# Optimization experiments

Measured on AMD Instinct MI355X. Metric: run time of the kernel, lower is better.

The kernel has to match this reference:

```python
import jax, jax.numpy as jnp
import numpy as np

N_NODES = 100_000
N_EDGES = 1_600_000
N_TOKENS = 16
VOCAB = 32_000
TOK_DIM = 64
NODE_DIM = 64
HID = 128
FC = 128
NUM_GRAPHS = 1024


def setup_inputs() -> dict:
    key = jax.random.key(0)
    ks = jax.random.split(key, 14)
    emb = jax.random.normal(ks[0], (VOCAB, TOK_DIM), jnp.float32) * 0.02
    emb = emb.at[0].set(0.0)  # padding_idx=0 row is zero
    return {
        "x_token_idxs": jax.random.randint(ks[1], (N_NODES, N_TOKENS), 0, VOCAB),
        "edge_index": jax.random.randint(ks[2], (2, N_EDGES), 0, N_NODES),
        "batch": jnp.sort(jax.random.randint(ks[3], (N_NODES,), 0, NUM_GRAPHS)),
        "emb": emb,
        "Wp": jax.random.normal(ks[4], (TOK_DIM, NODE_DIM), jnp.float32) * (1.0 / np.sqrt(TOK_DIM)),
        "bp": jnp.zeros((NODE_DIM,), jnp.float32),
        "W1": jax.random.normal(ks[5], (NODE_DIM, HID), jnp.float32) * (1.0 / np.sqrt(NODE_DIM)),
        "b1": jnp.zeros((HID,), jnp.float32),
        "W2": jax.random.normal(ks[6], (HID, HID), jnp.float32) * (1.0 / np.sqrt(HID)),
        "b2": jnp.zeros((HID,), jnp.float32),
        "Wfc": jax.random.normal(ks[7], (HID, FC), jnp.float32) * (1.0 / np.sqrt(HID)),
        "bfc": jnp.zeros((FC,), jnp.float32),
        "Wout": jax.random.normal(ks[8], (FC, 1), jnp.float32) * (1.0 / np.sqrt(FC)),
        "bout": jnp.zeros((1,), jnp.float32),
    }


def reference(x_token_idxs, edge_index, batch, emb, Wp, bp, W1, b1, W2, b2, Wfc, bfc, Wout, bout):
    N = x_token_idxs.shape[0]
    # token embed -> mean pool over tokens -> node projection
    node = emb[x_token_idxs].mean(axis=1) @ Wp + bp  # [N, NODE_DIM]

    # GCN normalization with self-loops (PyG gcn_norm, symmetric)
    loops = jnp.arange(N)
    src = jnp.concatenate([edge_index[0], loops])
    dst = jnp.concatenate([edge_index[1], loops])
    deg = jax.ops.segment_sum(jnp.ones_like(dst, jnp.float32), dst, num_segments=N)
    dis = jnp.where(deg > 0, jax.lax.rsqrt(deg), 0.0)
    norm = (dis[src] * dis[dst])[:, None]  # [E+N, 1]

    def gcn(x, W, b):
        h = x @ W                                      # linear transform first (in->out)
        msg = h[src] * norm                            # gather + scale
        return jax.ops.segment_sum(msg, dst, num_segments=N) + b  # scatter-add + bias

    x = jax.nn.relu(gcn(node, W1, b1))
    x = jax.nn.relu(gcn(x, W2, b2))

    # global mean pool by graph id
    cnt = jax.ops.segment_sum(jnp.ones((N,), jnp.float32), batch, num_segments=NUM_GRAPHS)
    g = jax.ops.segment_sum(x, batch, num_segments=NUM_GRAPHS) / jnp.maximum(cnt, 1.0)[:, None]

    g = jax.nn.relu(g @ Wfc + bfc)
    logits = (g @ Wout + bout).squeeze(-1)  # [NUM_GRAPHS]
    return jax.nn.sigmoid(logits), logits
```

## Files before the change

### kernel.cpp

```cpp
#include <hip/hip_runtime.h>
#include <hip/hip_bf16.h>
#include <hip/hip_fp16.h>
#include <math.h>

#define N_TOKENS 16
#define TOK_DIM 64
#define NODE_DIM 64
#define HID 128
#define FC 128
#define NUM_GRAPHS 1024
#define NBUCK_MAX 512
#define CHUNK 8192

typedef _Float16 f16x8 __attribute__((ext_vector_type(8)));
typedef float f32x4 __attribute__((ext_vector_type(4)));

__device__ __forceinline__ __half2 shfl_xor_h2(__half2 v, int mask) {
    int i = *(int*)&v;
    i = __shfl_xor(i, mask);
    return *(__half2*)&i;
}

__global__ void prep_weights_kernel(const float* __restrict__ Wp, const float* __restrict__ W1,
                                    const float* __restrict__ W2, const float* __restrict__ bp,
                                    _Float16* __restrict__ Wf16t, _Float16* __restrict__ W2t,
                                    float* __restrict__ bf) {
    int n = blockIdx.x;
    int t = threadIdx.x;
    if (t < 64) {
        float acc = 0.f;
#pragma unroll
        for (int d = 0; d < 64; d++) acc += Wp[t * 64 + d] * W1[d * 128 + n];
        Wf16t[(size_t)n * 64 + t] = (_Float16)acc;
    } else {
        int d = t - 64;
        float v = bp[d] * W1[d * 128 + n];
#pragma unroll
        for (int off = 32; off > 0; off >>= 1) v += __shfl_down(v, off);
        if (d == 0) bf[n] = v;
    }
    W2t[(size_t)n * 128 + t] = (_Float16)W2[(size_t)t * 128 + n];
}

__global__ void convert_emb_kernel(const float* __restrict__ emb, __half* __restrict__ emb16,
                                   int n4) {
    int i = blockIdx.x * 256 + threadIdx.x;
    if (i < n4) {
        float4 v = ((const float4*)emb)[i];
        __half2 h0 = __floats2half2_rn(v.x, v.y);
        __half2 h1 = __floats2half2_rn(v.z, v.w);
        float2 p;
        ((__half2*)&p)[0] = h0;
        ((__half2*)&p)[1] = h1;
        ((float2*)emb16)[i] = p;
    }
}

__global__ void embed_mean_kernel(const int* __restrict__ tok,
                                  const __half* __restrict__ emb16,
                                  __half* __restrict__ mean16, int N) {
    int t = threadIdx.x;
    int w = t >> 6, j = t & 63;
    int q = j >> 3, l = j & 7;
    int i = blockIdx.x * 4 + w;
    if (i >= N) return;
    const float4* e4 = (const float4*)emb16;
    int t0 = tok[i * 16 + q];
    int t1 = tok[i * 16 + q + 8];
    float4 v0 = e4[(size_t)t0 * 8 + l];
    float4 v1 = e4[(size_t)t1 * 8 + l];
    const __half2* p0 = (const __half2*)&v0;
    const __half2* p1 = (const __half2*)&v1;
    __half2 a0 = __hadd2(p0[0], p1[0]);
    __half2 a1 = __hadd2(p0[1], p1[1]);
    __half2 a2 = __hadd2(p0[2], p1[2]);
    __half2 a3 = __hadd2(p0[3], p1[3]);
#pragma unroll
    for (int mask = 8; mask <= 32; mask <<= 1) {
        a0 = __hadd2(a0, shfl_xor_h2(a0, mask));
        a1 = __hadd2(a1, shfl_xor_h2(a1, mask));
        a2 = __hadd2(a2, shfl_xor_h2(a2, mask));
        a3 = __hadd2(a3, shfl_xor_h2(a3, mask));
    }
    if (q == 0) {
        __half2 inv = __floats2half2_rn(1.0f / 16.0f, 1.0f / 16.0f);
        float4 packed;
        __half2* pp = (__half2*)&packed;
        pp[0] = __hmul2(a0, inv);
        pp[1] = __hmul2(a1, inv);
        pp[2] = __hmul2(a2, inv);
        pp[3] = __hmul2(a3, inv);
        ((float4*)mean16)[(size_t)i * 8 + l] = packed;
    }
}

__global__ void bucket_hist_kernel(const int* __restrict__ dst, int* __restrict__ bucket_cnt,
                                   int E, int nbuck) {
    __shared__ int h[NBUCK_MAX];
    int t = threadIdx.x;
    for (int i = t; i < nbuck; i += 512) h[i] = 0;
    __syncthreads();
    int base = blockIdx.x * CHUNK;
    for (int i = t; i < CHUNK; i += 512) {
        int e = base + i;
        if (e < E) atomicAdd(&h[dst[e] >> 8], 1);
    }
    __syncthreads();
    for (int i = t; i < nbuck; i += 512)
        if (h[i]) atomicAdd(&bucket_cnt[i], h[i]);
}

__global__ void bucket_scan_kernel(const int* __restrict__ bucket_cnt,
                                   int* __restrict__ bucket_base,
                                   int* __restrict__ bucket_cursor, int nbuck) {
    __shared__ int s[512];
    int tid = threadIdx.x;
    int v = (tid < nbuck) ? bucket_cnt[tid] : 0;
    s[tid] = v;
    __syncthreads();
    for (int off = 1; off < 512; off <<= 1) {
        int add = (tid >= off) ? s[tid - off] : 0;
        __syncthreads();
        s[tid] += add;
        __syncthreads();
    }
    if (tid < nbuck) { bucket_base[tid] = s[tid] - v; bucket_cursor[tid] = 0; }
    if (tid == 511) bucket_base[nbuck] = s[511];
}

__global__ void binscatter_kernel(const int* __restrict__ src, const int* __restrict__ dst,
                                  const int* __restrict__ bucket_base,
                                  int* __restrict__ bucket_cursor,
                                  int* __restrict__ staged, int E, int nbuck) {
    __shared__ int h[NBUCK_MAX];
    __shared__ int gw[NBUCK_MAX];
    int t = threadIdx.x;
    for (int i = t; i < nbuck; i += 512) h[i] = 0;
    __syncthreads();
    int base = blockIdx.x * CHUNK;
    for (int i = t; i < CHUNK; i += 512) {
        int e = base + i;
        if (e < E) atomicAdd(&h[dst[e] >> 8], 1);
    }
    __syncthreads();
    for (int i = t; i < nbuck; i += 512) {
        int c = h[i];
        gw[i] = (c > 0) ? bucket_base[i] + atomicAdd(&bucket_cursor[i], c) : 0;
        h[i] = 0;
    }
    __syncthreads();
    for (int i = t; i < CHUNK; i += 512) {
        int e = base + i;
        if (e < E) {
            int d = dst[e], s = src[e];
            int b = d >> 8;
            int r = atomicAdd(&h[b], 1);
            staged[gw[b] + r] = s | ((d & 255) << 17);
        }
    }
}

__global__ void bucket_count_kernel(const int* __restrict__ staged,
                                    const int* __restrict__ bucket_base,
                                    int* __restrict__ row_start, float* __restrict__ dis,
                                    int N, int E) {
    __shared__ int cnt[256];
    __shared__ int sc[256];
    int b = blockIdx.x;
    int t = threadIdx.x;
    cnt[t] = 0;
    __syncthreads();
    int rb0 = bucket_base[b], rb1 = bucket_base[b + 1];
    for (int i = rb0 + t; i < rb1; i += 256) atomicAdd(&cnt[staged[i] >> 17], 1);
    __syncthreads();
    int v = cnt[t];
    sc[t] = v;
    __syncthreads();
    for (int off = 1; off < 256; off <<= 1) {
        int add = (t >= off) ? sc[t - off] : 0;
        __syncthreads();
        sc[t] += add;
        __syncthreads();
    }
    int node = b * 256 + t;
    if (node < N) {
        row_start[node] = rb0 + sc[t] - v;
        dis[node] = rsqrtf(1.0f + (float)v);
    }
    if (b == 0 && t == 0) row_start[N] = E;
}

__global__ void csr_write_kernel(const int* __restrict__ staged,
                                 const int* __restrict__ bucket_base,
                                 const int* __restrict__ row_start,
                                 const float* __restrict__ dis,
                                 int2* __restrict__ csr, float* __restrict__ rowsum, int N) {
    __shared__ int cur[256];
    __shared__ float dl[256];
    __shared__ float wsum[256];
    int b = blockIdx.x;
    int t = threadIdx.x;
    int node = b * 256 + t;
    cur[t] = (node < N) ? row_start[node] : 0;
    dl[t] = (node < N) ? dis[node] : 0.f;
    wsum[t] = 0.f;
    __syncthreads();
    int rb0 = bucket_base[b], rb1 = bucket_base[b + 1];
    for (int i = rb0 + t; i < rb1; i += 256) {
        int v = staged[i];
        int s = v & 131071;
        int dloc = v >> 17;
        float w = dis[s] * dl[dloc];
        int pos = atomicAdd(&cur[dloc], 1);
        __half2 wh = __floats2half2_rn(w, w);
        csr[pos] = make_int2(s, *(int*)&wh);
        atomicAdd(&wsum[dloc], w);
    }
    __syncthreads();
    if (node < N) rowsum[node] = wsum[t] + dl[t] * dl[t];
}

__global__ __launch_bounds__(256, 8)
void agg64_kernel(const __half* __restrict__ mean16,
                  const int* __restrict__ row_start,
                  const int2* __restrict__ csr,
                  const float* __restrict__ dis,
                  __half* __restrict__ agg16, int N) {
    int t = threadIdx.x;
    int w = t >> 6, j = t & 63;
    int q = j >> 3, l = j & 7;
    int node = blockIdx.x * 4 + w;
    if (node >= N) return;
    int beg = row_start[node];
    int end = row_start[node + 1];
    float d = dis[node];
    const float4* m4 = (const float4*)mean16;
    __half2 a0, a1, a2, a3;
    {
        float4 raw = m4[(size_t)node * 8 + l];
        const __half2* hp = (const __half2*)&raw;
        float d2f = d * d * ((q == 0) ? 1.f : 0.f);
        __half2 d2h = __floats2half2_rn(d2f, d2f);
        a0 = __hmul2(hp[0], d2h); a1 = __hmul2(hp[1], d2h);
        a2 = __hmul2(hp[2], d2h); a3 = __hmul2(hp[3], d2h);
    }
    int k = beg;
    int kfull = beg + ((end - beg) & ~31);
    for (; k < kfull; k += 32) {
        int2 e[4];
        float4 v[4];
#pragma unroll
        for (int m = 0; m < 4; m++) e[m] = csr[k + 8 * m + q];
#pragma unroll
        for (int m = 0; m < 4; m++) v[m] = m4[(size_t)e[m].x * 8 + l];
#pragma unroll
        for (int m = 0; m < 4; m++) {
            __half2 wh = *(__half2*)&e[m].y;
            const __half2* hp = (const __half2*)&v[m];
            a0 = __hfma2(hp[0], wh, a0);
            a1 = __hfma2(hp[1], wh, a1);
            a2 = __hfma2(hp[2], wh, a2);
            a3 = __hfma2(hp[3], wh, a3);
        }
    }
    if (k < end) {
        int2 e[4];
        float4 v[4];
#pragma unroll
        for (int m = 0; m < 4; m++) {
            int kk = k + 8 * m + q;
            e[m] = (kk < end) ? csr[kk] : make_int2(0, 0);
        }
#pragma unroll
        for (int m = 0; m < 4; m++) v[m] = m4[(size_t)e[m].x * 8 + l];
#pragma unroll
        for (int m = 0; m < 4; m++) {
            __half2 wh = *(__half2*)&e[m].y;
            const __half2* hp = (const __half2*)&v[m];
            a0 = __hfma2(hp[0], wh, a0);
            a1 = __hfma2(hp[1], wh, a1);
            a2 = __hfma2(hp[2], wh, a2);
            a3 = __hfma2(hp[3], wh, a3);
        }
    }
#pragma unroll
    for (int mask = 8; mask <= 32; mask <<= 1) {
        a0 = __hadd2(a0, shfl_xor_h2(a0, mask));
        a1 = __hadd2(a1, shfl_xor_h2(a1, mask));
        a2 = __hadd2(a2, shfl_xor_h2(a2, mask));
        a3 = __hadd2(a3, shfl_xor_h2(a3, mask));
    }
    if (q == 0) {
        float4 packed;
        __half2* pp = (__half2*)&packed;
        pp[0] = a0; pp[1] = a1; pp[2] = a2; pp[3] = a3;
        ((float4*)agg16)[(size_t)node * 8 + l] = packed;
    }
}

#define NB 32
__global__ void dense_chain_mfma_kernel(const __half* __restrict__ agg16,
                                        const float* __restrict__ rowsum,
                                        const _Float16* __restrict__ Wf16t,
                                        const float* __restrict__ bf,
                                        const float* __restrict__ b1,
                                        const _Float16* __restrict__ W2t,
                                        __half* __restrict__ h2, int N) {
    __shared__ _Float16 sx1[32][136];
    __shared__ float srs[32];
    int t = threadIdx.x;
    int wv = t >> 6, lane = t & 63;
    int nb0 = blockIdx.x * NB;
    int rh = wv & 1;
    int ncb = (wv >> 1) * 64;
    int m16 = lane & 15;
    int q = lane >> 4;

    if (t < 32) srs[t] = (nb0 + t < N) ? rowsum[nb0 + t] : 0.f;

    f32x4 c0 = {}, c1 = {}, c2 = {}, c3 = {};
    int arow = nb0 + rh * 16 + m16;
    bool rowok = (arow < N);
    const _Float16* ag = (const _Float16*)agg16;
#pragma unroll
    for (int ks = 0; ks < 2; ks++) {
        int k0 = ks * 32 + q * 8;
        f16x8 afrag = {};
        if (rowok) afrag = *(const f16x8*)(ag + (size_t)arow * 64 + k0);
        f16x8 b0 = *(const f16x8*)(Wf16t + (size_t)(ncb + 0 * 16 + m16) * 64 + k0);
        f16x8 b1f = *(const f16x8*)(Wf16t + (size_t)(ncb + 1 * 16 + m16) * 64 + k0);
        f16x8 b2f = *(const f16x8*)(Wf16t + (size_t)(ncb + 2 * 16 + m16) * 64 + k0);
        f16x8 b3f = *(const f16x8*)(Wf16t + (size_t)(ncb + 3 * 16 + m16) * 64 + k0);
        c0 = __builtin_amdgcn_mfma_f32_16x16x32_f16(afrag, b0, c0, 0, 0, 0);
        c1 = __builtin_amdgcn_mfma_f32_16x16x32_f16(afrag, b1f, c1, 0, 0, 0);
        c2 = __builtin_amdgcn_mfma_f32_16x16x32_f16(afrag, b2f, c2, 0, 0, 0);
        c3 = __builtin_amdgcn_mfma_f32_16x16x32_f16(afrag, b3f, c3, 0, 0, 0);
    }
    __syncthreads();
    {
        f32x4 cc[4] = {c0, c1, c2, c3};
#pragma unroll
        for (int nt = 0; nt < 4; nt++) {
            int ncol = ncb + nt * 16 + m16;
            float bfj = bf[ncol], b1j = b1[ncol];
#pragma unroll
            for (int r = 0; r < 4; r++) {
                int mrow = q * 4 + r;
                float z = cc[nt][r] + srs[rh * 16 + mrow] * bfj + b1j;
                sx1[rh * 16 + mrow][ncol] = (_Float16)fmaxf(z, 0.f);
            }
        }
    }
    __syncthreads();

    f32x4 d0 = {}, d1 = {}, d2 = {}, d3 = {};
#pragma unroll
    for (int ks = 0; ks < 4; ks++) {
        int k0 = ks * 32 + q * 8;
        f16x8 afrag = *(const f16x8*)(&sx1[rh * 16 + m16][k0]);
        f16x8 b0 = *(const f16x8*)(W2t + (size_t)(ncb + 0 * 16 + m16) * 128 + k0);
        f16x8 b1f = *(const f16x8*)(W2t + (size_t)(ncb + 1 * 16 + m16) * 128 + k0);
        f16x8 b2f = *(const f16x8*)(W2t + (size_t)(ncb + 2 * 16 + m16) * 128 + k0);
        f16x8 b3f = *(const f16x8*)(W2t + (size_t)(ncb + 3 * 16 + m16) * 128 + k0);
        d0 = __builtin_amdgcn_mfma_f32_16x16x32_f16(afrag, b0, d0, 0, 0, 0);
        d1 = __builtin_amdgcn_mfma_f32_16x16x32_f16(afrag, b1f, d1, 0, 0, 0);
        d2 = __builtin_amdgcn_mfma_f32_16x16x32_f16(afrag, b2f, d2, 0, 0, 0);
        d3 = __builtin_amdgcn_mfma_f32_16x16x32_f16(afrag, b3f, d3, 0, 0, 0);
    }
    {
        f32x4 dd[4] = {d0, d1, d2, d3};
#pragma unroll
        for (int nt = 0; nt < 4; nt++) {
            int ncol = ncb + nt * 16 + m16;
#pragma unroll
            for (int r = 0; r < 4; r++) {
                int node = nb0 + rh * 16 + q * 4 + r;
                if (node < N) h2[(size_t)node * 128 + ncol] = __float2half(dd[nt][r]);
            }
        }
    }
}

__global__ __launch_bounds__(256, 8)
void gcn_agg128_kernel(const __half* __restrict__ hsrc,
                       const int* __restrict__ row_start,
                       const int2* __restrict__ csr,
                       const float* __restrict__ dis,
                       const float* __restrict__ b2,
                       __half* __restrict__ outx, int N) {
    int t = threadIdx.x;
    int w = t >> 6, j = t & 63;
    int q = j >> 4, l = j & 15;
    int node = blockIdx.x * 4 + w;
    if (node >= N) return;
    const float4* h4 = (const float4*)hsrc;
    int beg = row_start[node];
    int end = row_start[node + 1];
    float d = dis[node];
    __half2 a0, a1, a2, a3;
    {
        float4 raw = h4[(size_t)node * 16 + l];
        const __half2* hp = (const __half2*)&raw;
        float d2f = d * d * ((q == 0) ? 1.f : 0.f);
        __half2 d2h = __floats2half2_rn(d2f, d2f);
        a0 = __hmul2(hp[0], d2h); a1 = __hmul2(hp[1], d2h);
        a2 = __hmul2(hp[2], d2h); a3 = __hmul2(hp[3], d2h);
    }
    int k = beg;
    int kfull = beg + ((end - beg) & ~31);
    for (; k < kfull; k += 32) {
        int2 e[8];
        float4 v[8];
#pragma unroll
        for (int m = 0; m < 8; m++) e[m] = csr[k + 4 * m + q];
#pragma unroll
        for (int m = 0; m < 8; m++) v[m] = h4[(size_t)e[m].x * 16 + l];
#pragma unroll
        for (int m = 0; m < 8; m++) {
            __half2 wh = *(__half2*)&e[m].y;
            const __half2* hp = (const __half2*)&v[m];
            a0 = __hfma2(hp[0], wh, a0);
            a1 = __hfma2(hp[1], wh, a1);
            a2 = __hfma2(hp[2], wh, a2);
            a3 = __hfma2(hp[3], wh, a3);
        }
    }
    if (k < end) {
        int2 e[8];
        float4 v[8];
#pragma unroll
        for (int m = 0; m < 8; m++) {
            int kk = k + 4 * m + q;
            e[m] = (kk < end) ? csr[kk] : make_int2(0, 0);
        }
#pragma unroll
        for (int m = 0; m < 8; m++) v[m] = h4[(size_t)e[m].x * 16 + l];
#pragma unroll
        for (int m = 0; m < 8; m++) {
            __half2 wh = *(__half2*)&e[m].y;
            const __half2* hp = (const __half2*)&v[m];
            a0 = __hfma2(hp[0], wh, a0);
            a1 = __hfma2(hp[1], wh, a1);
            a2 = __hfma2(hp[2], wh, a2);
            a3 = __hfma2(hp[3], wh, a3);
        }
    }
#pragma unroll
    for (int mask = 16; mask <= 32; mask <<= 1) {
        a0 = __hadd2(a0, shfl_xor_h2(a0, mask));
        a1 = __hadd2(a1, shfl_xor_h2(a1, mask));
        a2 = __hadd2(a2, shfl_xor_h2(a2, mask));
        a3 = __hadd2(a3, shfl_xor_h2(a3, mask));
    }
    if (q == 0) {
        float2 f0 = __half22float2(a0), f1 = __half22float2(a1);
        float2 f2 = __half22float2(a2), f3 = __half22float2(a3);
        const float4* b4 = (const float4*)b2;
        float4 ba = b4[l * 2], bb = b4[l * 2 + 1];
        __half2 o0 = __floats2half2_rn(fmaxf(f0.x + ba.x, 0.f), fmaxf(f0.y + ba.y, 0.f));
        __half2 o1 = __floats2half2_rn(fmaxf(f1.x + ba.z, 0.f), fmaxf(f1.y + ba.w, 0.f));
        __half2 o2 = __floats2half2_rn(fmaxf(f2.x + bb.x, 0.f), fmaxf(f2.y + bb.y, 0.f));
        __half2 o3 = __floats2half2_rn(fmaxf(f3.x + bb.z, 0.f), fmaxf(f3.y + bb.w, 0.f));
        float4 packed;
        __half2* pp = (__half2*)&packed;
        pp[0] = o0; pp[1] = o1; pp[2] = o2; pp[3] = o3;
        ((float4*)outx)[(size_t)node * 16 + l] = packed;
    }
}

__device__ __forceinline__ int lower_bound_i(const int* __restrict__ a, int n, int val) {
    int lo = 0, hi = n;
    while (lo < hi) {
        int mid = (lo + hi) >> 1;
        if (a[mid] < val) lo = mid + 1; else hi = mid;
    }
    return lo;
}

__global__ void pool_head_kernel(const __half* __restrict__ x,
                                 const int* __restrict__ batch,
                                 const float* __restrict__ Wfc,
                                 const float* __restrict__ bfc,
                                 const float* __restrict__ Wout,
                                 const float* __restrict__ bout,
                                 float* __restrict__ out, int N) {
    int gr = blockIdx.x;
    int t = threadIdx.x;
    int j2 = t & 63, w = t >> 6;
    __shared__ float2 spart[2][64];
    __shared__ float sg[128];
    __shared__ float sred[128];
    int beg = lower_bound_i(batch, N, gr);
    int end = lower_bound_i(batch, N, gr + 1);
    const __half2* x2 = (const __half2*)x;
    float2 acc = make_float2(0.f, 0.f);
    for (int i = beg + w; i < end; i += 2) {
        float2 a = __half22float2(x2[(size_t)i * 64 + j2]);
        acc.x += a.x; acc.y += a.y;
    }
    spart[w][j2] = acc;
    __syncthreads();
    if (t < 64) {
        float inv = 1.0f / fmaxf((float)(end - beg), 1.0f);
        float2 s0 = spart[0][t], s1 = spart[1][t];
        sg[2 * t] = (s0.x + s1.x) * inv;
        sg[2 * t + 1] = (s0.y + s1.y) * inv;
    }
    __syncthreads();
    int j = t;
    float a = bfc[j];
#pragma unroll
    for (int k = 0; k < 128; k++) a += sg[k] * Wfc[k * 128 + j];
    float f = fmaxf(a, 0.f);
    sred[j] = f * Wout[j];
    __syncthreads();
    if (j < 64) sred[j] += sred[j + 64];
    __syncthreads();
    if (j < 64) {
        float v = sred[j];
#pragma unroll
        for (int off = 32; off > 0; off >>= 1) v += __shfl_down(v, off);
        if (j == 0) {
            float logit = v + bout[0];
            out[gr] = 1.0f / (1.0f + expf(-logit));
            out[NUM_GRAPHS + gr] = logit;
        }
    }
}

extern "C" void kernel_launch(void* const* d_in, const int* in_sizes, int n_in,
                              void* d_out, int out_size, void* d_ws, size_t ws_size,
                              hipStream_t stream) {
    const int* tok   = (const int*)d_in[0];
    const int* eidx  = (const int*)d_in[1];
    const int* batch = (const int*)d_in[2];
    const float* emb = (const float*)d_in[3];
    const float* Wp  = (const float*)d_in[4];
    const float* bp  = (const float*)d_in[5];
    const float* W1  = (const float*)d_in[6];
    const float* b1  = (const float*)d_in[7];
    const float* W2  = (const float*)d_in[8];
    const float* b2  = (const float*)d_in[9];
    const float* Wfc = (const float*)d_in[10];
    const float* bfc = (const float*)d_in[11];
    const float* Wout= (const float*)d_in[12];
    const float* bout= (const float*)d_in[13];
    float* out = (float*)d_out;

    const int N = in_sizes[2];
    const int E = in_sizes[1] / 2;
    const int* src = eidx;
    const int* dst = eidx + E;
    const int Np = (N + 3) & ~3;
    const int nbuck = (N + 255) / 256;
    const int nchunk = (E + CHUNK - 1) / CHUNK;
    const int emb_n4 = in_sizes[3] / 4;

    float* ws = (float*)d_ws;
    size_t off = 0;
    float* dis     = ws + off;            off += Np;
    __half* mean16 = (__half*)(ws + off); off += (size_t)Np * 32;
    __half* agg16  = (__half*)(ws + off); off += (size_t)Np * 32;
    float* rowsum  = ws + off;            off += Np;
    __half* h2buf  = (__half*)(ws + off); off += (size_t)Np * 64;
    __half* xfin16 = (__half*)(ws + off); off += (size_t)Np * 64;
    __half* emb16  = (__half*)(ws + off); off += (size_t)(in_sizes[3] / 2 + 4);
    _Float16* Wf16t = (_Float16*)(ws + off); off += 4096;
    _Float16* W2t   = (_Float16*)(ws + off); off += 8192;
    float* bf      = ws + off;            off += 128;
    int* row_start = (int*)(ws + off);    off += Np + 4;
    int* staged    = (int*)(ws + off);    off += E;
    int* bucket_cnt    = (int*)(ws + off); off += NBUCK_MAX;
    int* bucket_base   = (int*)(ws + off); off += NBUCK_MAX + 8;
    int* bucket_cursor = (int*)(ws + off); off += NBUCK_MAX;
    int2* csr      = (int2*)(ws + off);

    prep_weights_kernel<<<128, 128, 0, stream>>>(Wp, W1, W2, bp, Wf16t, W2t, bf);
    convert_emb_kernel<<<(emb_n4 + 255) / 256, 256, 0, stream>>>(emb, emb16, emb_n4);

    hipMemsetAsync(bucket_cnt, 0, nbuck * sizeof(int), stream);
    bucket_hist_kernel<<<nchunk, 512, 0, stream>>>(dst, bucket_cnt, E, nbuck);
    bucket_scan_kernel<<<1, 512, 0, stream>>>(bucket_cnt, bucket_base, bucket_cursor, nbuck);
    binscatter_kernel<<<nchunk, 512, 0, stream>>>(src, dst, bucket_base, bucket_cursor,
                                                  staged, E, nbuck);
    bucket_count_kernel<<<nbuck, 256, 0, stream>>>(staged, bucket_base, row_start, dis, N, E);
    csr_write_kernel<<<nbuck, 256, 0, stream>>>(staged, bucket_base, row_start, dis,
                                                csr, rowsum, N);

    embed_mean_kernel<<<(N + 3) / 4, 256, 0, stream>>>(tok, emb16, mean16, N);

    agg64_kernel<<<(N + 3) / 4, 256, 0, stream>>>(mean16, row_start, csr, dis, agg16, N);

    dense_chain_mfma_kernel<<<(N + NB - 1) / NB, 256, 0, stream>>>(agg16, rowsum, Wf16t,
                                                                   bf, b1, W2t, h2buf, N);

    gcn_agg128_kernel<<<(N + 3) / 4, 256, 0, stream>>>(h2buf, row_start, csr, dis, b2,
                                                       xfin16, N);

    pool_head_kernel<<<NUM_GRAPHS, 128, 0, stream>>>(xfin16, batch, Wfc, bfc, Wout, bout,
                                                     out, N);
}
```

Before: 349.3 us.

## Replace atomic bucket cursors with per-chunk histogram scan; widen pool head

```diff
diff --git a/kernel.cpp b/kernel.cpp
--- a/kernel.cpp
+++ b/kernel.cpp
@@ -94,7 +94,7 @@
     }
 }
 
-__global__ void bucket_hist_kernel(const int* __restrict__ dst, int* __restrict__ bucket_cnt,
+__global__ void bucket_hist_kernel(const int* __restrict__ dst, int* __restrict__ hist2d,
                                    int E, int nbuck) {
     __shared__ int h[NBUCK_MAX];
     int t = threadIdx.x;
@@ -106,16 +106,35 @@
         if (e < E) atomicAdd(&h[dst[e] >> 8], 1);
     }
     __syncthreads();
-    for (int i = t; i < nbuck; i += 512)
-        if (h[i]) atomicAdd(&bucket_cnt[i], h[i]);
-}
-
-__global__ void bucket_scan_kernel(const int* __restrict__ bucket_cnt,
-                                   int* __restrict__ bucket_base,
-                                   int* __restrict__ bucket_cursor, int nbuck) {
+    int* row = hist2d + (size_t)blockIdx.x * NBUCK_MAX;
+    for (int i = t; i < nbuck; i += 512) row[i] = h[i];
+}
+
+__global__ void chunk_scan_kernel(const int* __restrict__ hist2d, int* __restrict__ chunkbase,
+                                  int* __restrict__ total, int nchunk) {
+    int b = blockIdx.x;
+    int lane = threadIdx.x;
+    int run = 0;
+    for (int c0 = 0; c0 < nchunk; c0 += 64) {
+        int c = c0 + lane;
+        int v = (c < nchunk) ? hist2d[(size_t)c * NBUCK_MAX + b] : 0;
+        int s = v;
+#pragma unroll
+        for (int off = 1; off < 64; off <<= 1) {
+            int u = __shfl_up(s, off);
+            if (lane >= off) s += u;
+        }
+        if (c < nchunk) chunkbase[(size_t)c * NBUCK_MAX + b] = s - v + run;
+        run += __shfl(s, 63);
+    }
+    if (lane == 0) total[b] = run;
+}
+
+__global__ void bucket_scan_kernel(const int* __restrict__ total,
+                                   int* __restrict__ bucket_base, int nbuck) {
     __shared__ int s[512];
     int tid = threadIdx.x;
-    int v = (tid < nbuck) ? bucket_cnt[tid] : 0;
+    int v = (tid < nbuck) ? total[tid] : 0;
     s[tid] = v;
     __syncthreads();
     for (int off = 1; off < 512; off <<= 1) {
@@ -124,38 +143,27 @@
         s[tid] += add;
         __syncthreads();
     }
-    if (tid < nbuck) { bucket_base[tid] = s[tid] - v; bucket_cursor[tid] = 0; }
+    if (tid < nbuck) bucket_base[tid] = s[tid] - v;
     if (tid == 511) bucket_base[nbuck] = s[511];
 }
 
 __global__ void binscatter_kernel(const int* __restrict__ src, const int* __restrict__ dst,
                                   const int* __restrict__ bucket_base,
-                                  int* __restrict__ bucket_cursor,
+                                  const int* __restrict__ chunkbase,
                                   int* __restrict__ staged, int E, int nbuck) {
     __shared__ int h[NBUCK_MAX];
-    __shared__ int gw[NBUCK_MAX];
-    int t = threadIdx.x;
-    for (int i = t; i < nbuck; i += 512) h[i] = 0;
+    int t = threadIdx.x;
+    const int* cb = chunkbase + (size_t)blockIdx.x * NBUCK_MAX;
+    for (int i = t; i < nbuck; i += 512) h[i] = bucket_base[i] + cb[i];
     __syncthreads();
     int base = blockIdx.x * CHUNK;
-    for (int i = t; i < CHUNK; i += 512) {
-        int e = base + i;
-        if (e < E) atomicAdd(&h[dst[e] >> 8], 1);
-    }
-    __syncthreads();
-    for (int i = t; i < nbuck; i += 512) {
-        int c = h[i];
-        gw[i] = (c > 0) ? bucket_base[i] + atomicAdd(&bucket_cursor[i], c) : 0;
-        h[i] = 0;
-    }
-    __syncthreads();
     for (int i = t; i < CHUNK; i += 512) {
         int e = base + i;
         if (e < E) {
             int d = dst[e], s = src[e];
             int b = d >> 8;
             int r = atomicAdd(&h[b], 1);
-            staged[gw[b] + r] = s | ((d & 255) << 17);
+            staged[r] = s | ((d & 255) << 17);
         }
     }
 }
@@ -487,14 +495,15 @@
     int gr = blockIdx.x;
     int t = threadIdx.x;
     int j2 = t & 63, w = t >> 6;
-    __shared__ float2 spart[2][64];
+    __shared__ float2 spart[4][64];
     __shared__ float sg[128];
+    __shared__ float sfc[2][128];
     __shared__ float sred[128];
     int beg = lower_bound_i(batch, N, gr);
     int end = lower_bound_i(batch, N, gr + 1);
     const __half2* x2 = (const __half2*)x;
     float2 acc = make_float2(0.f, 0.f);
-    for (int i = beg + w; i < end; i += 2) {
+    for (int i = beg + w; i < end; i += 4) {
         float2 a = __half22float2(x2[(size_t)i * 64 + j2]);
         acc.x += a.x; acc.y += a.y;
     }
@@ -503,24 +512,28 @@
     if (t < 64) {
         float inv = 1.0f / fmaxf((float)(end - beg), 1.0f);
         float2 s0 = spart[0][t], s1 = spart[1][t];
-        sg[2 * t] = (s0.x + s1.x) * inv;
-        sg[2 * t + 1] = (s0.y + s1.y) * inv;
-    }
-    __syncthreads();
-    int j = t;
-    float a = bfc[j];
-#pragma unroll
-    for (int k = 0; k < 128; k++) a += sg[k] * Wfc[k * 128 + j];
-    float f = fmaxf(a, 0.f);
-    sred[j] = f * Wout[j];
-    __syncthreads();
-    if (j < 64) sred[j] += sred[j + 64];
-    __syncthreads();
-    if (j < 64) {
-        float v = sred[j];
+        float2 s2 = spart[2][t], s3 = spart[3][t];
+        sg[2 * t] = (s0.x + s1.x + s2.x + s3.x) * inv;
+        sg[2 * t + 1] = (s0.y + s1.y + s2.y + s3.y) * inv;
+    }
+    __syncthreads();
+    int j = t & 127, hb = t >> 7;
+    float a = 0.f;
+#pragma unroll
+    for (int k = 0; k < 64; k++) a += sg[hb * 64 + k] * Wfc[(hb * 64 + k) * 128 + j];
+    sfc[hb][j] = a;
+    __syncthreads();
+    if (t < 128) {
+        float aa = sfc[0][t] + sfc[1][t] + bfc[t];
+        float f = fmaxf(aa, 0.f);
+        sred[t] = f * Wout[t];
+    }
+    __syncthreads();
+    if (t < 64) {
+        float v = sred[t] + sred[t + 64];
 #pragma unroll
         for (int off = 32; off > 0; off >>= 1) v += __shfl_down(v, off);
-        if (j == 0) {
+        if (t == 0) {
             float logit = v + bout[0];
             out[gr] = 1.0f / (1.0f + expf(-logit));
             out[NUM_GRAPHS + gr] = logit;
@@ -570,18 +583,19 @@
     float* bf      = ws + off;            off += 128;
     int* row_start = (int*)(ws + off);    off += Np + 4;
     int* staged    = (int*)(ws + off);    off += E;
-    int* bucket_cnt    = (int*)(ws + off); off += NBUCK_MAX;
+    int* total     = (int*)(ws + off);    off += NBUCK_MAX;
     int* bucket_base   = (int*)(ws + off); off += NBUCK_MAX + 8;
-    int* bucket_cursor = (int*)(ws + off); off += NBUCK_MAX;
     int2* csr      = (int2*)(ws + off);
+    int* hist2d    = (int*)h2buf;
+    int* chunkbase = hist2d + (size_t)nchunk * NBUCK_MAX;
 
     prep_weights_kernel<<<128, 128, 0, stream>>>(Wp, W1, W2, bp, Wf16t, W2t, bf);
     convert_emb_kernel<<<(emb_n4 + 255) / 256, 256, 0, stream>>>(emb, emb16, emb_n4);
 
-    hipMemsetAsync(bucket_cnt, 0, nbuck * sizeof(int), stream);
-    bucket_hist_kernel<<<nchunk, 512, 0, stream>>>(dst, bucket_cnt, E, nbuck);
-    bucket_scan_kernel<<<1, 512, 0, stream>>>(bucket_cnt, bucket_base, bucket_cursor, nbuck);
-    binscatter_kernel<<<nchunk, 512, 0, stream>>>(src, dst, bucket_base, bucket_cursor,
+    bucket_hist_kernel<<<nchunk, 512, 0, stream>>>(dst, hist2d, E, nbuck);
+    chunk_scan_kernel<<<nbuck, 64, 0, stream>>>(hist2d, chunkbase, total, nchunk);
+    bucket_scan_kernel<<<1, 512, 0, stream>>>(total, bucket_base, nbuck);
+    binscatter_kernel<<<nchunk, 512, 0, stream>>>(src, dst, bucket_base, chunkbase,
                                                   staged, E, nbuck);
     bucket_count_kernel<<<nbuck, 256, 0, stream>>>(staged, bucket_base, row_start, dis, N, E);
     csr_write_kernel<<<nbuck, 256, 0, stream>>>(staged, bucket_base, row_start, dis,
@@ -597,6 +611,6 @@
     gcn_agg128_kernel<<<(N + 3) / 4, 256, 0, stream>>>(h2buf, row_start, csr, dis, b2,
                                                        xfin16, N);
 
-    pool_head_kernel<<<NUM_GRAPHS, 128, 0, stream>>>(xfin16, batch, Wfc, bfc, Wout, bout,
+    pool_head_kernel<<<NUM_GRAPHS, 256, 0, stream>>>(xfin16, batch, Wfc, bfc, Wout, bout,
                                                      out, N);
 }
```

After: 329.1 us. 5.8% less time.
